# Kernel tuning notes

Hardware: AMD Instinct MI355X
Metric: run time of the kernel (lower is better)

Reference implementation:

```python
import jax, jax.numpy as jnp
import numpy as np

B, S, D = 8, 2048, 512
DK = 64  # attention_dim

def setup_inputs() -> dict:
    key = jax.random.key(0)
    k0, k1, k2, k3 = jax.random.split(key, 4)
    inputs = jax.random.normal(k0, (B, S, D), dtype=jnp.float32)
    # add_weight initializer='random_normal' -> stddev 0.05 in keras
    W_q = jax.random.normal(k1, (D, DK), dtype=jnp.float32) * 0.05
    W_k = jax.random.normal(k2, (D, DK), dtype=jnp.float32) * 0.05
    W_v = jax.random.normal(k3, (D, DK), dtype=jnp.float32) * 0.05
    return {"inputs": inputs, "W_q": W_q, "W_k": W_k, "W_v": W_v}

def reference(inputs, W_q, W_k, W_v):
    # QKV projections: [B,S,D] @ [D,DK] -> [B,S,DK]
    q = jnp.einsum('bsd,dk->bsk', inputs, W_q)
    k = jnp.einsum('bsd,dk->bsk', inputs, W_k)
    v = jnp.einsum('bsd,dk->bsk', inputs, W_v)
    scale = 1.0 / jnp.sqrt(jnp.asarray(DK, dtype=q.dtype))
    scores = jnp.einsum('bqk,bsk->bqs', q, k) * scale  # [B,S,S]
    weights = jax.nn.softmax(scores, axis=-1)
    attended = jnp.einsum('bqs,bsk->bqk', weights, v)  # [B,S,DK]
    return attended, weights
```

## Files before the change

kernel.cpp:

```cpp
#include <hip/hip_runtime.h>


typedef __bf16 bf16x8 __attribute__((ext_vector_type(8)));
typedef float f32x4 __attribute__((ext_vector_type(4)));

__device__ __forceinline__ short f2bf(float f) {
    unsigned u = __builtin_bit_cast(unsigned, f);
    u = (u + 0x7fffu + ((u >> 16) & 1u)) >> 16;
    return (short)u;
}
__device__ __forceinline__ float bf2f(short h) {
    unsigned u = ((unsigned)(unsigned short)h) << 16;
    return __builtin_bit_cast(float, u);
}
__device__ __forceinline__ bf16x8 ldfrag(const short* p) {
    return *reinterpret_cast<const bf16x8*>(p);
}
__device__ __forceinline__ f32x4 mfma16(bf16x8 a, bf16x8 b, f32x4 c) {
    return __builtin_amdgcn_mfma_f32_16x16x32_bf16(a, b, c, 0, 0, 0);
}
__device__ __forceinline__ bf16x8 packbf8(f32x4 a, f32x4 b) {
    union { bf16x8 v; short s[8]; } u;
    #pragma unroll
    for (int i = 0; i < 4; i++) { u.s[i] = f2bf(a[i]); u.s[4 + i] = f2bf(b[i]); }
    return u.v;
}

__global__ void wtrans_kernel(const float* __restrict__ Wq,
                              const float* __restrict__ Wk,
                              const float* __restrict__ Wv,
                              short* __restrict__ wt_hi,
                              short* __restrict__ wt_lo) {
    int idx = blockIdx.x * 256 + threadIdx.x;
    int k = idx & 511;
    int n = (idx >> 9) & 63;
    int m = idx >> 15;
    const float* W = (m == 0) ? Wq : (m == 1) ? Wk : Wv;
    float w = W[k * 64 + n];
    short hi = f2bf(w);
    wt_hi[idx] = hi;
    if (m < 2) wt_lo[idx] = f2bf(w - bf2f(hi));
}

__global__ __launch_bounds__(256) void qkv_kernel(
    const float* __restrict__ x,
    const short* __restrict__ wt_hi, const short* __restrict__ wt_lo,
    short* __restrict__ Qg, short* __restrict__ Kg, short* __restrict__ VTg) {
  __shared__ __align__(16) short Ah[32 * 40], Al[32 * 40];
  __shared__ __align__(16) short Bqh[64 * 40], Bql[64 * 40];
  __shared__ __align__(16) short Bkh[64 * 40], Bkl[64 * 40];
  __shared__ __align__(16) short Bvh[64 * 40];
  const int t = threadIdx.x;
  const int wave = t >> 6, lane = t & 63, quad = lane >> 4, l15 = lane & 15;
  const int rg = wave & 1, ntp = wave >> 1;
  const int rbase = blockIdx.x * 32;

  f32x4 accq[2] = {}, acck[2] = {}, accv[2] = {};

  for (int k0 = 0; k0 < 512; k0 += 32) {
    {
      int row = t >> 3, off = (t & 7) << 2;
      float4 v = *(const float4*)(x + (size_t)(rbase + row) * 512 + k0 + off);
      short4 h, lo;
      h.x = f2bf(v.x); lo.x = f2bf(v.x - bf2f(h.x));
      h.y = f2bf(v.y); lo.y = f2bf(v.y - bf2f(h.y));
      h.z = f2bf(v.z); lo.z = f2bf(v.z - bf2f(h.z));
      h.w = f2bf(v.w); lo.w = f2bf(v.w - bf2f(h.w));
      *(short4*)(Ah + row * 40 + off) = h;
      *(short4*)(Al + row * 40 + off) = lo;
    }
    {
      int row = t >> 2, off = (t & 3) << 3;
      int src = row * 512 + k0 + off;
      int dst = row * 40 + off;
      *(int4*)(Bqh + dst) = *(const int4*)(wt_hi + 0 * 32768 + src);
      *(int4*)(Bkh + dst) = *(const int4*)(wt_hi + 1 * 32768 + src);
      *(int4*)(Bvh + dst) = *(const int4*)(wt_hi + 2 * 32768 + src);
      *(int4*)(Bql + dst) = *(const int4*)(wt_lo + 0 * 32768 + src);
      *(int4*)(Bkl + dst) = *(const int4*)(wt_lo + 1 * 32768 + src);
    }
    __syncthreads();
    bf16x8 ah = ldfrag(Ah + (rg * 16 + l15) * 40 + quad * 8);
    bf16x8 al = ldfrag(Al + (rg * 16 + l15) * 40 + quad * 8);
    #pragma unroll
    for (int j = 0; j < 2; j++) {
      const int nt = ntp * 2 + j;
      const int boff = (nt * 16 + l15) * 40 + quad * 8;
      bf16x8 bh = ldfrag(Bqh + boff);
      accq[j] = mfma16(ah, bh, accq[j]);
      accq[j] = mfma16(al, bh, accq[j]);
      accq[j] = mfma16(ah, ldfrag(Bql + boff), accq[j]);
      bh = ldfrag(Bkh + boff);
      acck[j] = mfma16(ah, bh, acck[j]);
      acck[j] = mfma16(al, bh, acck[j]);
      acck[j] = mfma16(ah, ldfrag(Bkl + boff), acck[j]);
      accv[j] = mfma16(ah, ldfrag(Bvh + boff), accv[j]);
    }
    __syncthreads();
  }
  #pragma unroll
  for (int j = 0; j < 2; j++) {
    const int nt = ntp * 2 + j;
    #pragma unroll
    for (int r = 0; r < 4; r++) {
      int row = rbase + rg * 16 + quad * 4 + r;
      int col = nt * 16 + l15;
      Qg[(size_t)row * 64 + col] = f2bf(accq[j][r]);
      Kg[(size_t)row * 64 + col] = f2bf(acck[j][r]);
    }
  }
  short* vt = Ah;
  #pragma unroll
  for (int j = 0; j < 2; j++) {
    const int col = (ntp * 2 + j) * 16 + l15;
    short4 p;
    p.x = f2bf(accv[j][0]); p.y = f2bf(accv[j][1]);
    p.z = f2bf(accv[j][2]); p.w = f2bf(accv[j][3]);
    *(short4*)(vt + col * 40 + rg * 16 + quad * 4) = p;
  }
  __syncthreads();
  {
    const int bidx = rbase >> 11;
    int c = t >> 2, ch = (t & 3) << 3;
    *(int4*)(VTg + (size_t)bidx * 131072 + (size_t)c * 2048 + (rbase & 2047) + ch) =
        *(const int4*)(vt + c * 40 + ch);
  }
}

__global__ __launch_bounds__(256) void attn_kernel(
    const short* __restrict__ Qg, const short* __restrict__ Kg,
    const short* __restrict__ VTg,
    float* __restrict__ att_out, float* __restrict__ w_out) {
  __shared__ __align__(16) short Qs[32 * 72];
  __shared__ __align__(16) short Ks[128 * 72];
  __shared__ __align__(16) short Vs[64 * 136];
  __shared__ __align__(16) float Pf[4][16 * 68];
  __shared__ float Lb[4][16];
  const int t = threadIdx.x;
  const int wave = t >> 6, lane = t & 63, quad = lane >> 4, l15 = lane & 15;
  const int rg = wave & 1, half = wave >> 1;
  const int b = blockIdx.x;
  const int qbase = blockIdx.y * 32;
  const float sc2 = 0.125f * 1.44269504088896340736f;
  const float C0 = 16.0f;

  {
    int row = t >> 3, off = (t & 7) << 3;
    *(int4*)(Qs + row * 72 + off) =
        *(const int4*)(Qg + (size_t)(b * 2048 + qbase + row) * 64 + off);
  }
  __syncthreads();
  const bf16x8 aq0 = ldfrag(Qs + (rg * 16 + l15) * 72 + quad * 8);
  const bf16x8 aq1 = ldfrag(Qs + (rg * 16 + l15) * 72 + 32 + quad * 8);

  float l[4] = {0.f, 0.f, 0.f, 0.f};

  for (int s0 = 0; s0 < 2048; s0 += 128) {
    #pragma unroll
    for (int i = 0; i < 4; i++) {
      int c = t + i * 256;
      int row = c >> 3, off = (c & 7) << 3;
      *(int4*)(Ks + row * 72 + off) =
          *(const int4*)(Kg + (size_t)(b * 2048 + s0 + row) * 64 + off);
    }
    __syncthreads();
    float ls[4] = {0.f, 0.f, 0.f, 0.f};
    #pragma unroll
    for (int nt2 = 0; nt2 < 4; nt2++) {
      const int nt = half * 4 + nt2;
      const int koff = (nt * 16 + l15) * 72 + quad * 8;
      f32x4 c = {};
      c = mfma16(aq0, ldfrag(Ks + koff), c);
      c = mfma16(aq1, ldfrag(Ks + koff + 32), c);
      #pragma unroll
      for (int r = 0; r < 4; r++) ls[r] += exp2f(c[r] * sc2 - C0);
    }
    #pragma unroll
    for (int r = 0; r < 4; r++) {
      float ps = ls[r];
      ps += __shfl_xor(ps, 1);
      ps += __shfl_xor(ps, 2);
      ps += __shfl_xor(ps, 4);
      ps += __shfl_xor(ps, 8);
      l[r] += ps;
    }
    __syncthreads();
  }
  if (l15 == 0) {
    #pragma unroll
    for (int r = 0; r < 4; r++) Lb[wave][quad * 4 + r] = l[r];
  }
  __syncthreads();
  float invl[4];
  #pragma unroll
  for (int r = 0; r < 4; r++)
    invl[r] = 1.0f / (Lb[wave][quad * 4 + r] + Lb[wave ^ 2][quad * 4 + r]);

  f32x4 acc[4] = {};
  float* wbase = w_out + ((size_t)b * 2048 + qbase + rg * 16) * 2048;

  for (int s0 = 0; s0 < 2048; s0 += 128) {
    #pragma unroll
    for (int i = 0; i < 4; i++) {
      int c = t + i * 256;
      int row = c >> 3, off = (c & 7) << 3;
      *(int4*)(Ks + row * 72 + off) =
          *(const int4*)(Kg + (size_t)(b * 2048 + s0 + row) * 64 + off);
    }
    #pragma unroll
    for (int i = 0; i < 4; i++) {
      int c = t + i * 256;
      int row = c >> 4, off = (c & 15) << 3;
      *(int4*)(Vs + row * 136 + off) =
          *(const int4*)(VTg + (size_t)b * 131072 + (size_t)row * 2048 + s0 + off);
    }
    __syncthreads();
    float* pf = Pf[wave];
    #pragma unroll
    for (int nt2 = 0; nt2 < 4; nt2++) {
      const int nt = half * 4 + nt2;
      const int koff = (nt * 16 + l15) * 72 + quad * 8;
      f32x4 c = {};
      c = mfma16(aq0, ldfrag(Ks + koff), c);
      c = mfma16(aq1, ldfrag(Ks + koff + 32), c);
      #pragma unroll
      for (int r = 0; r < 4; r++)
        pf[(quad * 4 + r) * 68 + nt2 * 16 + l15] =
            exp2f(c[r] * sc2 - C0) * invl[r];
    }
    #pragma unroll
    for (int i = 0; i < 4; i++) {
      int row = i * 4 + quad;
      f32x4 v = *(const f32x4*)(pf + row * 68 + l15 * 4);
      *(f32x4*)(wbase + (size_t)row * 2048 + s0 + half * 64 + l15 * 4) = v;
    }
    #pragma unroll
    for (int ks2 = 0; ks2 < 2; ks2++) {
      f32x4 p0 = *(const f32x4*)(pf + l15 * 68 + ks2 * 32 + quad * 8);
      f32x4 p1 = *(const f32x4*)(pf + l15 * 68 + ks2 * 32 + quad * 8 + 4);
      bf16x8 ap = packbf8(p0, p1);
      const int soff = half * 64 + ks2 * 32 + quad * 8;
      #pragma unroll
      for (int nc = 0; nc < 4; nc++)
        acc[nc] = mfma16(ap, ldfrag(Vs + (nc * 16 + l15) * 136 + soff), acc[nc]);
    }
    __syncthreads();
  }
  float* Ob = (float*)Pf;
  if (half == 1) {
    #pragma unroll
    for (int nc = 0; nc < 4; nc++)
      #pragma unroll
      for (int r = 0; r < 4; r++)
        Ob[(rg * 16 + quad * 4 + r) * 68 + nc * 16 + l15] = acc[nc][r];
  }
  __syncthreads();
  if (half == 0) {
    #pragma unroll
    for (int nc = 0; nc < 4; nc++)
      #pragma unroll
      for (int r = 0; r < 4; r++) {
        int row = rg * 16 + quad * 4 + r;
        att_out[((size_t)b * 2048 + qbase + row) * 64 + nc * 16 + l15] =
            acc[nc][r] + Ob[row * 68 + nc * 16 + l15];
      }
  }
}

extern "C" void kernel_launch(void* const* d_in, const int* in_sizes, int n_in,
                              void* d_out, int out_size, void* d_ws, size_t ws_size,
                              hipStream_t stream) {
  const float* x  = (const float*)d_in[0];
  const float* Wq = (const float*)d_in[1];
  const float* Wk = (const float*)d_in[2];
  const float* Wv = (const float*)d_in[3];

  char* ws = (char*)d_ws;
  short* wt_hi = (short*)(ws + 0);
  short* wt_lo = (short*)(ws + 196608);
  short* Qg    = (short*)(ws + 327680);
  short* Kg    = (short*)(ws + 327680 + 2097152);
  short* VTg   = (short*)(ws + 327680 + 4194304);

  float* att  = (float*)d_out;
  float* wout = att + (size_t)8 * 2048 * 64;

  hipLaunchKernelGGL(wtrans_kernel, dim3(384), dim3(256), 0, stream,
                     Wq, Wk, Wv, wt_hi, wt_lo);
  hipLaunchKernelGGL(qkv_kernel, dim3(512), dim3(256), 0, stream,
                     x, wt_hi, wt_lo, Qg, Kg, VTg);
  hipLaunchKernelGGL(attn_kernel, dim3(8, 64), dim3(256), 0, stream,
                     Qg, Kg, VTg, att, wout);
}
```

Before: 223.9 us.

## Register-prefetch next tiles of K, V, x and weights across loop iterations

Both the QKV projection and attention kernels now load the next iteration's global tiles into registers before computing on the current shared-memory tile, so global-load latency overlaps with MFMA work. The loop-closing barrier moves to the top of the next iteration. Launch bounds add a minimum of two blocks per CU. The cost is extra live registers for the prefetch buffers, which the occupancy hint may force into spills.

```diff
diff --git a/kernel.cpp b/kernel.cpp
--- a/kernel.cpp
+++ b/kernel.cpp
@@ -42,7 +42,7 @@
     if (m < 2) wt_lo[idx] = f2bf(w - bf2f(hi));
 }
 
-__global__ __launch_bounds__(256) void qkv_kernel(
+__global__ __launch_bounds__(256, 2) void qkv_kernel(
     const float* __restrict__ x,
     const short* __restrict__ wt_hi, const short* __restrict__ wt_lo,
     short* __restrict__ Qg, short* __restrict__ Kg, short* __restrict__ VTg) {
@@ -55,29 +55,49 @@
   const int rg = wave & 1, ntp = wave >> 1;
   const int rbase = blockIdx.x * 32;
 
+  const int row_a = t >> 3, off_a = (t & 7) << 2;
+  const int row_w = t >> 2, off_w = (t & 3) << 3;
+  const size_t xrow = (size_t)(rbase + row_a) * 512 + off_a;
+
   f32x4 accq[2] = {}, acck[2] = {}, accv[2] = {};
 
+  float4 xr;
+  int4 wr[5];
+  {
+    xr = *(const float4*)(x + xrow);
+    int src = row_w * 512 + off_w;
+    wr[0] = *(const int4*)(wt_hi + 0 * 32768 + src);
+    wr[1] = *(const int4*)(wt_hi + 1 * 32768 + src);
+    wr[2] = *(const int4*)(wt_hi + 2 * 32768 + src);
+    wr[3] = *(const int4*)(wt_lo + 0 * 32768 + src);
+    wr[4] = *(const int4*)(wt_lo + 1 * 32768 + src);
+  }
+
   for (int k0 = 0; k0 < 512; k0 += 32) {
+    if (k0) __syncthreads();
     {
-      int row = t >> 3, off = (t & 7) << 2;
-      float4 v = *(const float4*)(x + (size_t)(rbase + row) * 512 + k0 + off);
       short4 h, lo;
-      h.x = f2bf(v.x); lo.x = f2bf(v.x - bf2f(h.x));
-      h.y = f2bf(v.y); lo.y = f2bf(v.y - bf2f(h.y));
-      h.z = f2bf(v.z); lo.z = f2bf(v.z - bf2f(h.z));
-      h.w = f2bf(v.w); lo.w = f2bf(v.w - bf2f(h.w));
-      *(short4*)(Ah + row * 40 + off) = h;
-      *(short4*)(Al + row * 40 + off) = lo;
-    }
-    {
-      int row = t >> 2, off = (t & 3) << 3;
-      int src = row * 512 + k0 + off;
-      int dst = row * 40 + off;
-      *(int4*)(Bqh + dst) = *(const int4*)(wt_hi + 0 * 32768 + src);
-      *(int4*)(Bkh + dst) = *(const int4*)(wt_hi + 1 * 32768 + src);
-      *(int4*)(Bvh + dst) = *(const int4*)(wt_hi + 2 * 32768 + src);
-      *(int4*)(Bql + dst) = *(const int4*)(wt_lo + 0 * 32768 + src);
-      *(int4*)(Bkl + dst) = *(const int4*)(wt_lo + 1 * 32768 + src);
+      h.x = f2bf(xr.x); lo.x = f2bf(xr.x - bf2f(h.x));
+      h.y = f2bf(xr.y); lo.y = f2bf(xr.y - bf2f(h.y));
+      h.z = f2bf(xr.z); lo.z = f2bf(xr.z - bf2f(h.z));
+      h.w = f2bf(xr.w); lo.w = f2bf(xr.w - bf2f(h.w));
+      *(short4*)(Ah + row_a * 40 + off_a) = h;
+      *(short4*)(Al + row_a * 40 + off_a) = lo;
+      int dst = row_w * 40 + off_w;
+      *(int4*)(Bqh + dst) = wr[0];
+      *(int4*)(Bkh + dst) = wr[1];
+      *(int4*)(Bvh + dst) = wr[2];
+      *(int4*)(Bql + dst) = wr[3];
+      *(int4*)(Bkl + dst) = wr[4];
+    }
+    if (k0 + 32 < 512) {
+      xr = *(const float4*)(x + xrow + k0 + 32);
+      int src = row_w * 512 + k0 + 32 + off_w;
+      wr[0] = *(const int4*)(wt_hi + 0 * 32768 + src);
+      wr[1] = *(const int4*)(wt_hi + 1 * 32768 + src);
+      wr[2] = *(const int4*)(wt_hi + 2 * 32768 + src);
+      wr[3] = *(const int4*)(wt_lo + 0 * 32768 + src);
+      wr[4] = *(const int4*)(wt_lo + 1 * 32768 + src);
     }
     __syncthreads();
     bf16x8 ah = ldfrag(Ah + (rg * 16 + l15) * 40 + quad * 8);
@@ -96,8 +116,8 @@
       acck[j] = mfma16(ah, ldfrag(Bkl + boff), acck[j]);
       accv[j] = mfma16(ah, ldfrag(Bvh + boff), accv[j]);
     }
-    __syncthreads();
-  }
+  }
+  __syncthreads();
   #pragma unroll
   for (int j = 0; j < 2; j++) {
     const int nt = ntp * 2 + j;
@@ -127,7 +147,7 @@
   }
 }
 
-__global__ __launch_bounds__(256) void attn_kernel(
+__global__ __launch_bounds__(256, 2) void attn_kernel(
     const short* __restrict__ Qg, const short* __restrict__ Kg,
     const short* __restrict__ VTg,
     float* __restrict__ att_out, float* __restrict__ w_out) {
@@ -144,6 +164,11 @@
   const float sc2 = 0.125f * 1.44269504088896340736f;
   const float C0 = 16.0f;
 
+  const int krow0 = t >> 3, koff = (t & 7) << 3;
+  const int vrow0 = t >> 4, voff = (t & 15) << 3;
+  const short* Kb = Kg + (size_t)b * 131072;
+  const short* Vb = VTg + (size_t)b * 131072;
+
   {
     int row = t >> 3, off = (t & 7) << 3;
     *(int4*)(Qs + row * 72 + off) =
@@ -154,24 +179,30 @@
   const bf16x8 aq1 = ldfrag(Qs + (rg * 16 + l15) * 72 + 32 + quad * 8);
 
   float l[4] = {0.f, 0.f, 0.f, 0.f};
-
+  int4 kr[4], vr[4];
+
+  #pragma unroll
+  for (int i = 0; i < 4; i++)
+    kr[i] = *(const int4*)(Kb + (size_t)(krow0 + i * 32) * 64 + koff);
   for (int s0 = 0; s0 < 2048; s0 += 128) {
-    #pragma unroll
-    for (int i = 0; i < 4; i++) {
-      int c = t + i * 256;
-      int row = c >> 3, off = (c & 7) << 3;
-      *(int4*)(Ks + row * 72 + off) =
-          *(const int4*)(Kg + (size_t)(b * 2048 + s0 + row) * 64 + off);
+    if (s0) __syncthreads();
+    #pragma unroll
+    for (int i = 0; i < 4; i++)
+      *(int4*)(Ks + (krow0 + i * 32) * 72 + koff) = kr[i];
+    if (s0 + 128 < 2048) {
+      #pragma unroll
+      for (int i = 0; i < 4; i++)
+        kr[i] = *(const int4*)(Kb + (size_t)(s0 + 128 + krow0 + i * 32) * 64 + koff);
     }
     __syncthreads();
     float ls[4] = {0.f, 0.f, 0.f, 0.f};
     #pragma unroll
     for (int nt2 = 0; nt2 < 4; nt2++) {
       const int nt = half * 4 + nt2;
-      const int koff = (nt * 16 + l15) * 72 + quad * 8;
+      const int koff2 = (nt * 16 + l15) * 72 + quad * 8;
       f32x4 c = {};
-      c = mfma16(aq0, ldfrag(Ks + koff), c);
-      c = mfma16(aq1, ldfrag(Ks + koff + 32), c);
+      c = mfma16(aq0, ldfrag(Ks + koff2), c);
+      c = mfma16(aq1, ldfrag(Ks + koff2 + 32), c);
       #pragma unroll
       for (int r = 0; r < 4; r++) ls[r] += exp2f(c[r] * sc2 - C0);
     }
@@ -184,8 +215,8 @@
       ps += __shfl_xor(ps, 8);
       l[r] += ps;
     }
-    __syncthreads();
-  }
+  }
+  __syncthreads();
   if (l15 == 0) {
     #pragma unroll
     for (int r = 0; r < 4; r++) Lb[wave][quad * 4 + r] = l[r];
@@ -199,30 +230,34 @@
   f32x4 acc[4] = {};
   float* wbase = w_out + ((size_t)b * 2048 + qbase + rg * 16) * 2048;
 
+  #pragma unroll
+  for (int i = 0; i < 4; i++) {
+    kr[i] = *(const int4*)(Kb + (size_t)(krow0 + i * 32) * 64 + koff);
+    vr[i] = *(const int4*)(Vb + (size_t)(vrow0 + i * 16) * 2048 + voff);
+  }
   for (int s0 = 0; s0 < 2048; s0 += 128) {
+    if (s0) __syncthreads();
     #pragma unroll
     for (int i = 0; i < 4; i++) {
-      int c = t + i * 256;
-      int row = c >> 3, off = (c & 7) << 3;
-      *(int4*)(Ks + row * 72 + off) =
-          *(const int4*)(Kg + (size_t)(b * 2048 + s0 + row) * 64 + off);
-    }
-    #pragma unroll
-    for (int i = 0; i < 4; i++) {
-      int c = t + i * 256;
-      int row = c >> 4, off = (c & 15) << 3;
-      *(int4*)(Vs + row * 136 + off) =
-          *(const int4*)(VTg + (size_t)b * 131072 + (size_t)row * 2048 + s0 + off);
+      *(int4*)(Ks + (krow0 + i * 32) * 72 + koff) = kr[i];
+      *(int4*)(Vs + (vrow0 + i * 16) * 136 + voff) = vr[i];
+    }
+    if (s0 + 128 < 2048) {
+      #pragma unroll
+      for (int i = 0; i < 4; i++) {
+        kr[i] = *(const int4*)(Kb + (size_t)(s0 + 128 + krow0 + i * 32) * 64 + koff);
+        vr[i] = *(const int4*)(Vb + (size_t)(vrow0 + i * 16) * 2048 + s0 + 128 + voff);
+      }
     }
     __syncthreads();
     float* pf = Pf[wave];
     #pragma unroll
     for (int nt2 = 0; nt2 < 4; nt2++) {
       const int nt = half * 4 + nt2;
-      const int koff = (nt * 16 + l15) * 72 + quad * 8;
+      const int koff2 = (nt * 16 + l15) * 72 + quad * 8;
       f32x4 c = {};
-      c = mfma16(aq0, ldfrag(Ks + koff), c);
-      c = mfma16(aq1, ldfrag(Ks + koff + 32), c);
+      c = mfma16(aq0, ldfrag(Ks + koff2), c);
+      c = mfma16(aq1, ldfrag(Ks + koff2 + 32), c);
       #pragma unroll
       for (int r = 0; r < 4; r++)
         pf[(quad * 4 + r) * 68 + nt2 * 16 + l15] =
@@ -244,8 +279,8 @@
       for (int nc = 0; nc < 4; nc++)
         acc[nc] = mfma16(ap, ldfrag(Vs + (nc * 16 + l15) * 136 + soff), acc[nc]);
     }
-    __syncthreads();
-  }
+  }
+  __syncthreads();
   float* Ob = (float*)Pf;
   if (half == 1) {
     #pragma unroll
```

Measured after the change: 280.7 us. 25.4% more time.
